# Performance work log

Hardware: AMD Instinct MI355X
Metric: run time of the kernel (lower is better)

## Reference

```python
import jax, jax.numpy as jnp
import numpy as np

B = 8192          # batch
LATENT = 32       # latent_dim
H = 64            # hidden_size
SEQ_LEN = 180
NUM_CLASSES = 6
IN = 2            # GRU input size (zeros) / output features


def setup_inputs() -> dict:
    key = jax.random.key(0)
    ks = jax.random.split(key, 12)
    s_fc = 1.0 / np.sqrt(LATENT + H)
    s_rnn = 1.0 / np.sqrt(H)
    return {
        "z": jax.random.normal(ks[0], (B, LATENT), dtype=jnp.float32),
        "labels": jax.random.randint(ks[1], (B,), 0, NUM_CLASSES),
        "embed_w": jax.random.normal(ks[2], (NUM_CLASSES, H), dtype=jnp.float32),
        "fc_w": jax.random.uniform(ks[3], (H, LATENT + H), jnp.float32, -s_fc, s_fc),
        "fc_b": jax.random.uniform(ks[4], (H,), jnp.float32, -s_fc, s_fc),
        "w_ih": jax.random.uniform(ks[5], (3 * H, IN), jnp.float32, -s_rnn, s_rnn),
        "w_hh": jax.random.uniform(ks[6], (3 * H, H), jnp.float32, -s_rnn, s_rnn),
        "b_ih": jax.random.uniform(ks[7], (3 * H,), jnp.float32, -s_rnn, s_rnn),
        "b_hh": jax.random.uniform(ks[8], (3 * H,), jnp.float32, -s_rnn, s_rnn),
        "out_w": jax.random.uniform(ks[9], (IN, H), jnp.float32, -s_rnn, s_rnn),
        "out_b": jax.random.uniform(ks[10], (IN,), jnp.float32, -s_rnn, s_rnn),
    }


def reference(z, labels, embed_w, fc_w, fc_b, w_ih, w_hh, b_ih, b_hh, out_w, out_b):
    # h0 = tanh(fc([z, embed(labels)]))  -> [B, H]
    cond = embed_w[labels]
    h0 = jnp.tanh(jnp.concatenate([z, cond], axis=1) @ fc_w.T + fc_b)

    # GRU input is all zeros, so the input-side gates are constant per step:
    # gi = x_t @ w_ih.T + b_ih = b_ih  (kept faithful to torch GRU math)
    i_r, i_z, i_n = jnp.split(b_ih, 3)

    def step(h, _):
        gh = h @ w_hh.T + b_hh                      # [B, 3H]
        h_r, h_z, h_n = jnp.split(gh, 3, axis=-1)
        r = jax.nn.sigmoid(i_r + h_r)
        zg = jax.nn.sigmoid(i_z + h_z)
        n = jnp.tanh(i_n + r * h_n)
        h_new = (1.0 - zg) * n + zg * h
        return h_new, h_new

    _, hs = jax.lax.scan(step, h0, None, length=SEQ_LEN)  # [S, B, H]
    # out linear: [B, S, 2]
    return jnp.einsum("sbh,oh->bso", hs, out_w) + out_b
```

## Files before the change

kernel.cpp:

```cpp
#include <hip/hip_runtime.h>

#define NB     8192
#define HDIM   64
#define SEQ    180
#define MT     16
#define SB     72
#define XSP    100

typedef __bf16 bf16x8 __attribute__((ext_vector_type(8)));
typedef float  f32x4  __attribute__((ext_vector_type(4)));

#define L2E 1.44269504088896340736f

__device__ __forceinline__ float tanh_f(float x) {
    float e = __builtin_amdgcn_exp2f((2.0f * L2E) * x);
    return 1.0f - 2.0f * __builtin_amdgcn_rcpf(1.0f + e);
}

#define MFMA __builtin_amdgcn_mfma_f32_16x16x32_bf16

__global__ __launch_bounds__(256) void gru_all(
        const float* __restrict__ z, const int* __restrict__ labels,
        const float* __restrict__ embed_w, const float* __restrict__ fc_w,
        const float* __restrict__ fc_b, const float* __restrict__ w_hh,
        const float* __restrict__ b_ih, const float* __restrict__ b_hh,
        const float* __restrict__ out_w, const float* __restrict__ out_b,
        float* __restrict__ out) {
    __shared__ __align__(16) __bf16 hbuf[2][MT * SB];
    __shared__ __align__(16) float  xs[MT * XSP];

    const int t = threadIdx.x;
    const int w = t >> 6;
    const int l = t & 63;
    const int q = l >> 4;
    const int n16 = l & 15;
    const int jg = 16 * w + n16;
    const int bbase = blockIdx.x * MT;

    for (int c = t; c < MT * 24; c += 256) {
        int m = c / 24, kk = (c % 24) * 4;
        f32x4 v;
        if (kk < 32) v = *(const f32x4*)(z + (size_t)(bbase + m) * 32 + kk);
        else         v = *(const f32x4*)(embed_w + labels[bbase + m] * 64 + (kk - 32));
        *(f32x4*)(xs + m * XSP + kk) = v;
    }

    bf16x8 whi[3][2];
#pragma unroll
    for (int g = 0; g < 3; ++g) {
        const float* pr = w_hh + (g * 64 + jg) * HDIM;
#pragma unroll
        for (int ks = 0; ks < 2; ++ks) {
            const float* p = pr + ks * 32 + q * 8;
            f32x4 va = *(const f32x4*)(p);
            f32x4 vb = *(const f32x4*)(p + 4);
#pragma unroll
            for (int j2 = 0; j2 < 4; ++j2) {
                whi[g][ks][j2]     = (__bf16)va[j2];
                whi[g][ks][4 + j2] = (__bf16)vb[j2];
            }
        }
    }

    bf16x8 obhi[2];
#pragma unroll
    for (int ks = 0; ks < 2; ++ks) {
        f32x4 va = {0.f, 0.f, 0.f, 0.f}, vb = {0.f, 0.f, 0.f, 0.f};
        if (n16 < 2) {
            va = *(const f32x4*)(out_w + n16 * 64 + ks * 32 + q * 8);
            vb = *(const f32x4*)(out_w + n16 * 64 + ks * 32 + q * 8 + 4);
        }
#pragma unroll
        for (int j2 = 0; j2 < 4; ++j2) {
            obhi[ks][j2]     = (__bf16)va[j2];
            obhi[ks][4 + j2] = (__bf16)vb[j2];
        }
    }
    const float bo = (n16 == 0) ? out_b[0] : (n16 == 1) ? out_b[1] : 0.f;
    const f32x4 obias = {bo, bo, bo, bo};
    const f32x4 kZ = {0.f, 0.f, 0.f, 0.f};
    const f32x4 one4 = {1.f, 1.f, 1.f, 1.f};

    const float cR = -L2E * (b_ih[jg] + b_hh[jg]);
    const float cZ = -L2E * (b_ih[64 + jg] + b_hh[64 + jg]);
    const float bn = b_hh[128 + jg];
    const float cN = 2.0f * L2E * b_ih[128 + jg];
    const f32x4 cR4 = {cR, cR, cR, cR};
    const f32x4 cZ4 = {cZ, cZ, cZ, cZ};
    const f32x4 bn4 = {bn, bn, bn, bn};
    const f32x4 cN4 = {cN, cN, cN, cN};

    const int rdoff = n16 * SB + q * 8;
    const int wroff = (4 * q) * SB + jg;
    float* oph = out + (size_t)(bbase + 4 * q) * (SEQ * 2) + n16;

    __syncthreads();

    f32x4 hprev;
    {
        float a[4];
#pragma unroll
        for (int r = 0; r < 4; ++r) a[r] = fc_b[jg];
        const float* wr = fc_w + jg * 96;
        for (int kc = 0; kc < 24; ++kc) {
            f32x4 wv = *(const f32x4*)(wr + kc * 4);
#pragma unroll
            for (int r = 0; r < 4; ++r) {
                f32x4 xv = *(const f32x4*)(xs + (4 * q + r) * XSP + kc * 4);
                a[r] += wv[0] * xv[0] + wv[1] * xv[1] + wv[2] * xv[2] + wv[3] * xv[3];
            }
        }
#pragma unroll
        for (int r = 0; r < 4; ++r) {
            float h = tanh_f(a[r]);
            hprev[r] = h;
            hbuf[0][wroff + r * SB] = (__bf16)h;
        }
    }
    __syncthreads();

    if ((blockIdx.x >> 8) & 1) __builtin_amdgcn_s_sleep(8);

    for (int u = 0; u < SEQ / 4; ++u) {
#pragma unroll
        for (int s = 0; s < 4; ++s) {
            const int p = s & 1;
            const __bf16* Hh = hbuf[p];
            __bf16* Nh = hbuf[1 - p];

            bf16x8 ahi0 = *(const bf16x8*)(Hh + rdoff);
            bf16x8 ahi1 = *(const bf16x8*)(Hh + rdoff + 32);

            if ((u | s) != 0 && w == ((s + 3) & 3)) {
                f32x4 o = obias;
                o = MFMA(ahi0, obhi[0], o, 0, 0, 0);
                o = MFMA(ahi1, obhi[1], o, 0, 0, 0);
                if (n16 < 2) {
#pragma unroll
                    for (int r = 0; r < 4; ++r)
                        oph[r * (SEQ * 2) + 2 * s - 2] = o[r];
                }
            }

            f32x4 aR, aZ, aN;
            aR = MFMA(ahi0, whi[0][0], kZ, 0, 0, 0);
            aZ = MFMA(ahi0, whi[1][0], kZ, 0, 0, 0);
            aN = MFMA(ahi0, whi[2][0], kZ, 0, 0, 0);
            aR = MFMA(ahi1, whi[0][1], aR, 0, 0, 0);
            aZ = MFMA(ahi1, whi[1][1], aZ, 0, 0, 0);
            aN = MFMA(ahi1, whi[2][1], aN, 0, 0, 0);

            f32x4 tR = aR * (-L2E) + cR4;
            f32x4 tZ = aZ * (-L2E) + cZ4;
            f32x4 eR, eZ;
#pragma unroll
            for (int r = 0; r < 4; ++r) {
                eR[r] = __builtin_amdgcn_exp2f(tR[r]);
                eZ[r] = __builtin_amdgcn_exp2f(tZ[r]);
            }
            eR = eR + one4;
            eZ = eZ + one4;
            f32x4 rg, zg;
#pragma unroll
            for (int r = 0; r < 4; ++r) {
                rg[r] = __builtin_amdgcn_rcpf(eR[r]);
                zg[r] = __builtin_amdgcn_rcpf(eZ[r]);
            }
            f32x4 mm = aN + bn4;
            f32x4 tN = (rg * mm) * (2.0f * L2E) + cN4;
            f32x4 eN;
#pragma unroll
            for (int r = 0; r < 4; ++r) eN[r] = __builtin_amdgcn_exp2f(tN[r]);
            eN = eN + one4;
            f32x4 dd;
#pragma unroll
            for (int r = 0; r < 4; ++r) dd[r] = __builtin_amdgcn_rcpf(eN[r]);
            f32x4 ng = dd * (-2.0f) + one4;
            f32x4 hn = zg * (hprev - ng) + ng;
            hprev = hn;
#pragma unroll
            for (int r = 0; r < 4; ++r)
                Nh[wroff + r * SB] = (__bf16)hn[r];

            __syncthreads();
        }
        oph += 8;
    }

    if (w == 3) {
        const __bf16* Hh = hbuf[0];
        bf16x8 ahi0 = *(const bf16x8*)(Hh + rdoff);
        bf16x8 ahi1 = *(const bf16x8*)(Hh + rdoff + 32);
        f32x4 o = obias;
        o = MFMA(ahi0, obhi[0], o, 0, 0, 0);
        o = MFMA(ahi1, obhi[1], o, 0, 0, 0);
        if (n16 < 2) {
#pragma unroll
            for (int r = 0; r < 4; ++r)
                oph[r * (SEQ * 2) - 2] = o[r];
        }
    }
}

extern "C" void kernel_launch(void* const* d_in, const int* in_sizes, int n_in,
                              void* d_out, int out_size, void* d_ws, size_t ws_size,
                              hipStream_t stream) {
    (void)in_sizes; (void)n_in; (void)out_size; (void)d_ws; (void)ws_size;
    const float* z       = (const float*)d_in[0];
    const int*   labels  = (const int*)d_in[1];
    const float* embed_w = (const float*)d_in[2];
    const float* fc_w    = (const float*)d_in[3];
    const float* fc_b    = (const float*)d_in[4];
    const float* w_hh    = (const float*)d_in[6];
    const float* b_ih    = (const float*)d_in[7];
    const float* b_hh    = (const float*)d_in[8];
    const float* out_w   = (const float*)d_in[9];
    const float* out_b   = (const float*)d_in[10];
    float* out = (float*)d_out;

    gru_all<<<NB / MT, 256, 0, stream>>>(z, labels, embed_w, fc_w, fc_b,
                                         w_hh, b_ih, b_hh, out_w, out_b, out);
}
```

Measured before the change: 180.9 us.

## Halve batch rows per block to double grid size and cut per-step gate work

Each block now handles 8 batch rows instead of 16, so twice as many blocks are launched. The MFMA tile keeps 16 rows, but only the even-numbered rows are real; the rest are zeroed padding. Each lane now runs gate math on 2 values instead of 4, which shortens the serial per-step latency and spreads the recurrence over more CUs. In exchange, half of the MFMA throughput is spent on padding, and the block start staggering becomes a four-level sleep pattern.

```diff
diff --git a/kernel.cpp b/kernel.cpp
--- a/kernel.cpp
+++ b/kernel.cpp
@@ -3,12 +3,13 @@
 #define NB     8192
 #define HDIM   64
 #define SEQ    180
-#define MT     16
+#define MT     8
 #define SB     72
 #define XSP    100
 
 typedef __bf16 bf16x8 __attribute__((ext_vector_type(8)));
 typedef float  f32x4  __attribute__((ext_vector_type(4)));
+typedef float  f32x2  __attribute__((ext_vector_type(2)));
 
 #define L2E 1.44269504088896340736f
 
@@ -26,7 +27,7 @@
         const float* __restrict__ b_ih, const float* __restrict__ b_hh,
         const float* __restrict__ out_w, const float* __restrict__ out_b,
         float* __restrict__ out) {
-    __shared__ __align__(16) __bf16 hbuf[2][MT * SB];
+    __shared__ __align__(16) __bf16 hbuf[2][16 * SB];
     __shared__ __align__(16) float  xs[MT * XSP];
 
     const int t = threadIdx.x;
@@ -37,6 +38,9 @@
     const int jg = 16 * w + n16;
     const int bbase = blockIdx.x * MT;
 
+    for (int c = t; c < 2 * 16 * SB / 2; c += 256)
+        ((unsigned int*)hbuf)[c] = 0u;
+
     for (int c = t; c < MT * 24; c += 256) {
         int m = c / 24, kk = (c % 24) * 4;
         f32x4 v;
@@ -79,47 +83,47 @@
     const float bo = (n16 == 0) ? out_b[0] : (n16 == 1) ? out_b[1] : 0.f;
     const f32x4 obias = {bo, bo, bo, bo};
     const f32x4 kZ = {0.f, 0.f, 0.f, 0.f};
-    const f32x4 one4 = {1.f, 1.f, 1.f, 1.f};
+    const f32x2 one2 = {1.f, 1.f};
 
     const float cR = -L2E * (b_ih[jg] + b_hh[jg]);
     const float cZ = -L2E * (b_ih[64 + jg] + b_hh[64 + jg]);
     const float bn = b_hh[128 + jg];
     const float cN = 2.0f * L2E * b_ih[128 + jg];
-    const f32x4 cR4 = {cR, cR, cR, cR};
-    const f32x4 cZ4 = {cZ, cZ, cZ, cZ};
-    const f32x4 bn4 = {bn, bn, bn, bn};
-    const f32x4 cN4 = {cN, cN, cN, cN};
+    const f32x2 cR2 = {cR, cR};
+    const f32x2 cZ2 = {cZ, cZ};
+    const f32x2 bn2 = {bn, bn};
+    const f32x2 cN2 = {cN, cN};
 
     const int rdoff = n16 * SB + q * 8;
-    const int wroff = (4 * q) * SB + jg;
-    float* oph = out + (size_t)(bbase + 4 * q) * (SEQ * 2) + n16;
+    const int wr0 = (4 * q) * SB + jg;
+    const int wr1 = (4 * q + 2) * SB + jg;
+    float* oph = out + (size_t)(bbase + 2 * q) * (SEQ * 2) + n16;
 
     __syncthreads();
 
-    f32x4 hprev;
+    f32x2 hprev;
     {
-        float a[4];
-#pragma unroll
-        for (int r = 0; r < 4; ++r) a[r] = fc_b[jg];
+        float a0 = fc_b[jg], a1 = a0;
         const float* wr = fc_w + jg * 96;
         for (int kc = 0; kc < 24; ++kc) {
             f32x4 wv = *(const f32x4*)(wr + kc * 4);
-#pragma unroll
-            for (int r = 0; r < 4; ++r) {
-                f32x4 xv = *(const f32x4*)(xs + (4 * q + r) * XSP + kc * 4);
-                a[r] += wv[0] * xv[0] + wv[1] * xv[1] + wv[2] * xv[2] + wv[3] * xv[3];
-            }
-        }
-#pragma unroll
-        for (int r = 0; r < 4; ++r) {
-            float h = tanh_f(a[r]);
-            hprev[r] = h;
-            hbuf[0][wroff + r * SB] = (__bf16)h;
-        }
+            f32x4 x0 = *(const f32x4*)(xs + (2 * q) * XSP + kc * 4);
+            f32x4 x1 = *(const f32x4*)(xs + (2 * q + 1) * XSP + kc * 4);
+            a0 += wv[0] * x0[0] + wv[1] * x0[1] + wv[2] * x0[2] + wv[3] * x0[3];
+            a1 += wv[0] * x1[0] + wv[1] * x1[1] + wv[2] * x1[2] + wv[3] * x1[3];
+        }
+        hprev[0] = tanh_f(a0);
+        hprev[1] = tanh_f(a1);
+        hbuf[0][wr0] = (__bf16)hprev[0];
+        hbuf[0][wr1] = (__bf16)hprev[1];
     }
     __syncthreads();
 
-    if ((blockIdx.x >> 8) & 1) __builtin_amdgcn_s_sleep(8);
+    {
+        int k = (blockIdx.x >> 8) & 3;
+        if (k & 1) __builtin_amdgcn_s_sleep(3);
+        if (k & 2) __builtin_amdgcn_s_sleep(6);
+    }
 
     for (int u = 0; u < SEQ / 4; ++u) {
 #pragma unroll
@@ -136,9 +140,8 @@
                 o = MFMA(ahi0, obhi[0], o, 0, 0, 0);
                 o = MFMA(ahi1, obhi[1], o, 0, 0, 0);
                 if (n16 < 2) {
-#pragma unroll
-                    for (int r = 0; r < 4; ++r)
-                        oph[r * (SEQ * 2) + 2 * s - 2] = o[r];
+                    oph[2 * s - 2]       = o[0];
+                    oph[360 + 2 * s - 2] = o[2];
                 }
             }
 
@@ -150,37 +153,39 @@
             aZ = MFMA(ahi1, whi[1][1], aZ, 0, 0, 0);
             aN = MFMA(ahi1, whi[2][1], aN, 0, 0, 0);
 
-            f32x4 tR = aR * (-L2E) + cR4;
-            f32x4 tZ = aZ * (-L2E) + cZ4;
-            f32x4 eR, eZ;
-#pragma unroll
-            for (int r = 0; r < 4; ++r) {
+            f32x2 vR = {aR[0], aR[2]};
+            f32x2 vZ = {aZ[0], aZ[2]};
+            f32x2 vN = {aN[0], aN[2]};
+            f32x2 tR = vR * (-L2E) + cR2;
+            f32x2 tZ = vZ * (-L2E) + cZ2;
+            f32x2 eR, eZ;
+#pragma unroll
+            for (int r = 0; r < 2; ++r) {
                 eR[r] = __builtin_amdgcn_exp2f(tR[r]);
                 eZ[r] = __builtin_amdgcn_exp2f(tZ[r]);
             }
-            eR = eR + one4;
-            eZ = eZ + one4;
-            f32x4 rg, zg;
-#pragma unroll
-            for (int r = 0; r < 4; ++r) {
+            eR = eR + one2;
+            eZ = eZ + one2;
+            f32x2 rg, zg;
+#pragma unroll
+            for (int r = 0; r < 2; ++r) {
                 rg[r] = __builtin_amdgcn_rcpf(eR[r]);
                 zg[r] = __builtin_amdgcn_rcpf(eZ[r]);
             }
-            f32x4 mm = aN + bn4;
-            f32x4 tN = (rg * mm) * (2.0f * L2E) + cN4;
-            f32x4 eN;
-#pragma unroll
-            for (int r = 0; r < 4; ++r) eN[r] = __builtin_amdgcn_exp2f(tN[r]);
-            eN = eN + one4;
-            f32x4 dd;
-#pragma unroll
-            for (int r = 0; r < 4; ++r) dd[r] = __builtin_amdgcn_rcpf(eN[r]);
-            f32x4 ng = dd * (-2.0f) + one4;
-            f32x4 hn = zg * (hprev - ng) + ng;
+            f32x2 mm = vN + bn2;
+            f32x2 tN = (rg * mm) * (2.0f * L2E) + cN2;
+            f32x2 eN;
+#pragma unroll
+            for (int r = 0; r < 2; ++r) eN[r] = __builtin_amdgcn_exp2f(tN[r]);
+            eN = eN + one2;
+            f32x2 dd;
+#pragma unroll
+            for (int r = 0; r < 2; ++r) dd[r] = __builtin_amdgcn_rcpf(eN[r]);
+            f32x2 ng = dd * (-2.0f) + one2;
+            f32x2 hn = zg * (hprev - ng) + ng;
             hprev = hn;
-#pragma unroll
-            for (int r = 0; r < 4; ++r)
-                Nh[wroff + r * SB] = (__bf16)hn[r];
+            Nh[wr0] = (__bf16)hn[0];
+            Nh[wr1] = (__bf16)hn[1];
 
             __syncthreads();
         }
@@ -195,9 +200,8 @@
         o = MFMA(ahi0, obhi[0], o, 0, 0, 0);
         o = MFMA(ahi1, obhi[1], o, 0, 0, 0);
         if (n16 < 2) {
-#pragma unroll
-            for (int r = 0; r < 4; ++r)
-                oph[r * (SEQ * 2) - 2] = o[r];
+            oph[-2]       = o[0];
+            oph[358]      = o[2];
         }
     }
 }
```

New measurement: 200.7 us. +11.0%, slower.
